# Kernel tuning notes

Hardware: AMD Instinct MI355X
Metric: run time of the kernel (lower is better)

Reference implementation:

```python
import jax, jax.numpy as jnp
import numpy as np

HID = 100

def _make_params(key):
    dims = [(2, HID), (HID, HID), (HID, HID), (HID, HID), (HID, 2)]
    params = {}
    for i, (fan_in, fan_out) in enumerate(dims):
        k1, k2, key = jax.random.split(key, 3)
        bound = 1.0 / np.sqrt(fan_in)
        params[f"W{i+1}"] = jax.random.uniform(k1, (fan_out, fan_in), jnp.float32, -bound, bound)
        params[f"b{i+1}"] = jax.random.uniform(k2, (fan_out,), jnp.float32, -bound, bound)
    return params

def setup_inputs() -> dict:
    key = jax.random.key(0)
    kx, kt, kp = jax.random.split(key, 3)
    N = 262144
    inp = {
        "x": jax.random.normal(kx, (N, 1), jnp.float32),
        "t": jax.random.uniform(kt, (N, 1), jnp.float32),
    }
    inp.update(_make_params(kp))
    return inp

def reference(x, t, W1, b1, W2, b2, W3, b3, W4, b4, W5, b5):
    hidden = [(W1, b1), (W2, b2), (W3, b3), (W4, b4)]

    def u(xs, ts):  # scalar xs, ts -> [2] = (u_r, u_i)
        h = jnp.stack([xs, ts])
        for W, b in hidden:
            h = jnp.tanh(W @ h + b)
        return W5 @ h + b5

    u_t = jax.jacfwd(u, argnums=1)          # [2]: (u_t_r, u_t_i)
    u_x = jax.jacfwd(u, argnums=0)          # [2]
    u_xx = jax.jacfwd(u_x, argnums=0)       # [2]: (u_xx_r, u_xx_i)

    def per_point(xs, ts):
        return u(xs, ts), u_t(xs, ts), u_xx(xs, ts)

    U, Ut, Uxx = jax.vmap(per_point)(x[:, 0], t[:, 0])  # each [N, 2]

    u_r, u_i = U[:, 0:1], U[:, 1:2]
    u_t_r, u_t_i = Ut[:, 0:1], Ut[:, 1:2]
    u_xx_r, u_xx_i = Uxx[:, 0:1], Uxx[:, 1:2]

    mag2 = u_r * u_r + u_i * u_i
    f_r = -u_t_i + 0.5 * u_xx_r + mag2 * u_r
    f_i = u_t_r + 0.5 * u_xx_i + mag2 * u_i
    return f_r, f_i
```

## Files before the change

### kernel.cpp

```cpp
#include <hip/hip_runtime.h>


using half8 = __attribute__((ext_vector_type(8))) _Float16;
using half4 = __attribute__((ext_vector_type(4))) _Float16;
using f32x4 = __attribute__((ext_vector_type(4))) float;

#define LW      44800
#define ZOFF    134400
#define STGOFF  134416
#define STGW    2304
#define PLANEB  1152
#define NWAVES  12
#define SMEM_BYTES 162064

union U8 { uint4 u; half8 h; };
union U4 { uint2 u; half4 h; };

static __device__ __forceinline__ float fast_tanh(float z) {
    float e = __expf(2.0f * z);
    return 1.0f - 2.0f * __builtin_amdgcn_rcpf(e + 1.0f);
}

static __device__ __forceinline__ void split2(float v, _Float16& h0, _Float16& h1) {
    h0 = (_Float16)v;
    h1 = (_Float16)((v - (float)h0) * 512.0f);
}

__global__ void prep_w(const float* __restrict__ W2, const float* __restrict__ W3,
                       const float* __restrict__ W4, unsigned short* __restrict__ ws) {
    int bid = blockIdx.x;
    int l = bid / 28, rem = bid % 28, kt = rem / 7, jt = rem % 7;
    const float* W = (l == 0) ? W2 : (l == 1) ? W3 : W4;
    int lane = threadIdx.x;
    int c = lane & 15, q = lane >> 4;
    int j = 16 * jt + c;
    if (kt < 3) {
        for (int s = 0; s < 2; ++s)
            for (int i = 0; i < 8; ++i) {
                int k = 32 * kt + 8 * q + i;
                float w = (j < 100) ? W[j * 100 + k] : 0.0f;
                _Float16 h0 = (_Float16)w;
                _Float16 val = (s == 0) ? h0 : (_Float16)((w - (float)h0) * 512.0f);
                ws[(l*LW + kt*14336 + jt*2048 + s*1024 + lane*16 + i*2) >> 1] =
                    __builtin_bit_cast(unsigned short, val);
            }
    } else if (lane < 16) {
        for (int s = 0; s < 2; ++s)
            for (int i = 0; i < 4; ++i) {
                int k = 96 + i;
                float w = (j < 100) ? W[j * 100 + k] : 0.0f;
                _Float16 h0 = (_Float16)w;
                _Float16 val = (s == 0) ? h0 : (_Float16)((w - (float)h0) * 512.0f);
                ws[(l*LW + 43008 + jt*256 + s*128 + lane*8 + i*2) >> 1] =
                    __builtin_bit_cast(unsigned short, val);
            }
    }
}

__global__ void __launch_bounds__(768) pinn_mfma(
    const float* __restrict__ x,  const float* __restrict__ t,
    const float* __restrict__ W1, const float* __restrict__ b1,
    const float* __restrict__ b2, const float* __restrict__ b3,
    const float* __restrict__ b4,
    const float* __restrict__ W5, const float* __restrict__ b5,
    const char* __restrict__ ws, float* __restrict__ out,
    int N, int nchunks)
{
    extern __shared__ char smem[];
    const int tid  = threadIdx.x;
    const int w    = tid >> 6;
    const int lane = tid & 63;
    const int c15  = lane & 15;
    const int q    = lane >> 4;

    for (int it = 0; it < 11; ++it) {
        int idx = tid + it * 768;
        if (idx < 8400) ((uint4*)smem)[idx] = ((const uint4*)ws)[idx];
    }
    if (tid < 4) *(unsigned*)(smem + ZOFF + tid * 4) = 0u;
    __syncthreads();

    char* stg = smem + STGOFF + w * STGW;

    half8 a0[3], a1[3];
    half4 a0t,   a1t;
    f32x4 c0[7], c1[7];

    for (int chunk = blockIdx.x; chunk < nchunks; chunk += gridDim.x) {
        const int colbase = chunk * 192 + w * 16;

        {
            int col = colbase + c15;
            int pt = col >> 2, ch = col & 3;
            int ptc = (pt < N) ? pt : (N - 1);
            float xv = x[ptc], tv = t[ptc];
            #pragma unroll
            for (int kt = 0; kt < 3; ++kt) {
                half8 v0, v1;
                #pragma unroll
                for (int i = 0; i < 8; ++i) {
                    int j = 32 * kt + 8 * q + i;
                    float w0 = W1[2*j], w1 = W1[2*j+1], bb = b1[j];
                    float p = fmaf(w0, xv, fmaf(w1, tv, bb));
                    float a = fast_tanh(p);
                    float s = 1.0f - a * a;
                    float v = (ch == 0) ? a : (ch == 1) ? s * w1
                             : (ch == 2) ? s * w0 : -2.0f * a * s * w0 * w0;
                    _Float16 h0, h1; split2(v, h0, h1);
                    v0[i] = h0; v1[i] = h1;
                }
                a0[kt] = v0; a1[kt] = v1;
            }
            half4 t0 = {0, 0, 0, 0}, t1 = {0, 0, 0, 0};
            if (q == 0) {
                #pragma unroll
                for (int i = 0; i < 4; ++i) {
                    int j = 96 + i;
                    float w0 = W1[2*j], w1 = W1[2*j+1], bb = b1[j];
                    float p = fmaf(w0, xv, fmaf(w1, tv, bb));
                    float a = fast_tanh(p);
                    float s = 1.0f - a * a;
                    float v = (ch == 0) ? a : (ch == 1) ? s * w1
                             : (ch == 2) ? s * w0 : -2.0f * a * s * w0 * w0;
                    _Float16 h0, h1; split2(v, h0, h1);
                    t0[i] = h0; t1[i] = h1;
                }
            }
            a0t = t0; a1t = t1;
        }

        for (int l = 0; l < 3; ++l) {
            const char* WL = smem + l * LW;
            const float* BL = (l == 0) ? b2 : (l == 1) ? b3 : b4;

            #pragma unroll
            for (int jt = 0; jt < 7; ++jt) {
                c0[jt] = (f32x4){0.f, 0.f, 0.f, 0.f};
                c1[jt] = (f32x4){0.f, 0.f, 0.f, 0.f};
            }

            #pragma unroll
            for (int kt = 0; kt < 3; ++kt)
                #pragma unroll
                for (int jt = 0; jt < 7; ++jt) {
                    U8 b0u, b1u;
                    b0u.u = *(const uint4*)(WL + kt*14336 + jt*2048 + lane*16);
                    b1u.u = *(const uint4*)(WL + kt*14336 + jt*2048 + 1024 + lane*16);
                    c0[jt] = __builtin_amdgcn_mfma_f32_16x16x32_f16(a0[kt], b0u.h, c0[jt], 0, 0, 0);
                    c1[jt] = __builtin_amdgcn_mfma_f32_16x16x32_f16(a0[kt], b1u.h, c1[jt], 0, 0, 0);
                    c1[jt] = __builtin_amdgcn_mfma_f32_16x16x32_f16(a1[kt], b0u.h, c1[jt], 0, 0, 0);
                }
            #pragma unroll
            for (int jt = 0; jt < 7; ++jt) {
                int toff  = (lane < 16) ? (l*LW + 43008 + jt*256 + lane*8) : ZOFF;
                int toff1 = (lane < 16) ? (toff + 128) : ZOFF;
                U4 b0u, b1u;
                b0u.u = *(const uint2*)(smem + toff);
                b1u.u = *(const uint2*)(smem + toff1);
                c0[jt] = __builtin_amdgcn_mfma_f32_16x16x16f16(a0t, b0u.h, c0[jt], 0, 0, 0);
                c1[jt] = __builtin_amdgcn_mfma_f32_16x16x16f16(a0t, b1u.h, c1[jt], 0, 0, 0);
                c1[jt] = __builtin_amdgcn_mfma_f32_16x16x16f16(a1t, b0u.h, c1[jt], 0, 0, 0);
            }

            if (l < 2) {
                #pragma unroll
                for (int kc = 0; kc < 4; ++kc) {
                    int njt = (kc < 3) ? 2 : 1;
                    #pragma unroll
                    for (int jj = 0; jj < 2; ++jj) {
                        if (jj >= njt) continue;
                        int jt = 2 * kc + jj;
                        int kk = 16 * jj + c15;
                        int j  = 16 * jt + c15;
                        float bj = BL[(j < 100) ? j : 99];
                        float z0 = c0[jt][0] + c1[jt][0] * (1.0f/512.0f) + bj;
                        float z1 = c0[jt][1] + c1[jt][1] * (1.0f/512.0f);
                        float z2 = c0[jt][2] + c1[jt][2] * (1.0f/512.0f);
                        float z3 = c0[jt][3] + c1[jt][3] * (1.0f/512.0f);
                        float a = fast_tanh(z0);
                        float s = 1.0f - a * a;
                        float v[4];
                        v[0] = a; v[1] = s * z1; v[2] = s * z2;
                        v[3] = fmaf(-2.0f * a * s * z2, z2, s * z3);
                        #pragma unroll
                        for (int r = 0; r < 4; ++r) {
                            _Float16 h0, h1; split2(v[r], h0, h1);
                            _Float16* bp = (_Float16*)(stg) + (4 * q + r) * 36 + kk;
                            bp[0]   = h0;
                            bp[576] = h1;
                        }
                    }
                    if (kc < 3) {
                        const char* rb = stg + c15 * 72 + 16 * q;
                        U8 u;
                        uint2 L, H;
                        L = *(const uint2*)(rb);              H = *(const uint2*)(rb + 8);
                        u.u = (uint4){L.x, L.y, H.x, H.y};    a0[kc] = u.h;
                        L = *(const uint2*)(rb + PLANEB);     H = *(const uint2*)(rb + PLANEB + 8);
                        u.u = (uint4){L.x, L.y, H.x, H.y};    a1[kc] = u.h;
                    } else {
                        U4 u;
                        if (q == 0) {
                            const char* rb = stg + c15 * 72;
                            u.u = *(const uint2*)(rb);            a0t = u.h;
                            u.u = *(const uint2*)(rb + PLANEB);   a1t = u.h;
                        } else {
                            a0t = (half4){0,0,0,0}; a1t = (half4){0,0,0,0};
                        }
                    }
                }
            } else {
                float p00 = 0.f, p01 = 0.f, p03 = 0.f;
                float p10 = 0.f, p11 = 0.f, p13 = 0.f;
                #pragma unroll
                for (int jt = 0; jt < 7; ++jt) {
                    int j = 16 * jt + c15;
                    int j2 = (j < 100) ? j : 99;
                    float m = (j < 100) ? 1.0f : 0.0f;
                    float bj = BL[j2];
                    float w50 = W5[j2] * m, w51 = W5[100 + j2] * m;
                    float z0 = c0[jt][0] + c1[jt][0] * (1.0f/512.0f) + bj;
                    float z1 = c0[jt][1] + c1[jt][1] * (1.0f/512.0f);
                    float z2 = c0[jt][2] + c1[jt][2] * (1.0f/512.0f);
                    float z3 = c0[jt][3] + c1[jt][3] * (1.0f/512.0f);
                    float a = fast_tanh(z0);
                    float s = 1.0f - a * a;
                    float v0 = a, v1 = s * z1;
                    float v3 = fmaf(-2.0f * a * s * z2, z2, s * z3);
                    p00 = fmaf(w50, v0, p00);
                    p01 = fmaf(w50, v1, p01);
                    p03 = fmaf(w50, v3, p03);
                    p10 = fmaf(w51, v0, p10);
                    p11 = fmaf(w51, v1, p11);
                    p13 = fmaf(w51, v3, p13);
                }
                #pragma unroll
                for (int m = 1; m <= 8; m <<= 1) {
                    p00 += __shfl_xor(p00, m, 64);
                    p01 += __shfl_xor(p01, m, 64);
                    p03 += __shfl_xor(p03, m, 64);
                    p10 += __shfl_xor(p10, m, 64);
                    p11 += __shfl_xor(p11, m, 64);
                    p13 += __shfl_xor(p13, m, 64);
                }
                int pt = chunk * 48 + w * 4 + q;
                if (c15 == 0 && pt < N) {
                    float ur = p00 + b5[0], ui = p10 + b5[1];
                    float mag2 = ur * ur + ui * ui;
                    float fr = fmaf(mag2, ur, fmaf(0.5f, p03, -p11));
                    float fi = fmaf(mag2, ui, fmaf(0.5f, p13,  p01));
                    out[pt]     = fr;
                    out[N + pt] = fi;
                }
            }
        }
    }
}

extern "C" void kernel_launch(void* const* d_in, const int* in_sizes, int n_in,
                              void* d_out, int out_size, void* d_ws, size_t ws_size,
                              hipStream_t stream) {
    const float* x  = (const float*)d_in[0];
    const float* t  = (const float*)d_in[1];
    const float* W1 = (const float*)d_in[2];
    const float* b1 = (const float*)d_in[3];
    const float* W2 = (const float*)d_in[4];
    const float* b2 = (const float*)d_in[5];
    const float* W3 = (const float*)d_in[6];
    const float* b3 = (const float*)d_in[7];
    const float* W4 = (const float*)d_in[8];
    const float* b4 = (const float*)d_in[9];
    const float* W5 = (const float*)d_in[10];
    const float* b5 = (const float*)d_in[11];
    float* out = (float*)d_out;
    const int N = in_sizes[0];
    const int nchunks = (N + 47) / 48;

    (void)hipFuncSetAttribute((const void*)pinn_mfma,
                              hipFuncAttributeMaxDynamicSharedMemorySize, SMEM_BYTES);

    prep_w<<<84, 64, 0, stream>>>(W2, W3, W4, (unsigned short*)d_ws);
    pinn_mfma<<<256, 768, SMEM_BYTES, stream>>>(x, t, W1, b1, b2, b3, b4, W5, b5,
                                                (const char*)d_ws, out, N, nchunks);
}
```

Before: 436.1 us.

## Read MFMA weights directly from global memory instead of staging in LDS

Removes the per-block copy of all three hidden-layer weight matrices (about 134 KB) into shared memory. MFMA B operands are now loaded straight from the global workspace, relying on L1/L2 caching. Blocks shrink from 12 waves to 4, and the launch grows to 2048 blocks with an occupancy hint, so more independent waves can hide load latency. The cost is more global/cache traffic per MFMA and possible L1 thrashing, since every wave repeatedly reloads the same weights.

```diff
diff --git a/kernel.cpp b/kernel.cpp
--- a/kernel.cpp
+++ b/kernel.cpp
@@ -6,12 +6,9 @@
 using f32x4 = __attribute__((ext_vector_type(4))) float;
 
 #define LW      44800
-#define ZOFF    134400
-#define STGOFF  134416
 #define STGW    2304
 #define PLANEB  1152
-#define NWAVES  12
-#define SMEM_BYTES 162064
+#define NWAVES  4
 
 union U8 { uint4 u; half8 h; };
 union U4 { uint2 u; half4 h; };
@@ -57,7 +54,7 @@
     }
 }
 
-__global__ void __launch_bounds__(768) pinn_mfma(
+__global__ void __launch_bounds__(256, 5) pinn_mfma(
     const float* __restrict__ x,  const float* __restrict__ t,
     const float* __restrict__ W1, const float* __restrict__ b1,
     const float* __restrict__ b2, const float* __restrict__ b3,
@@ -66,28 +63,21 @@
     const char* __restrict__ ws, float* __restrict__ out,
     int N, int nchunks)
 {
-    extern __shared__ char smem[];
+    __shared__ __align__(16) char smem[NWAVES * STGW];
     const int tid  = threadIdx.x;
     const int w    = tid >> 6;
     const int lane = tid & 63;
     const int c15  = lane & 15;
     const int q    = lane >> 4;
 
-    for (int it = 0; it < 11; ++it) {
-        int idx = tid + it * 768;
-        if (idx < 8400) ((uint4*)smem)[idx] = ((const uint4*)ws)[idx];
-    }
-    if (tid < 4) *(unsigned*)(smem + ZOFF + tid * 4) = 0u;
-    __syncthreads();
-
-    char* stg = smem + STGOFF + w * STGW;
+    char* stg = smem + w * STGW;
 
     half8 a0[3], a1[3];
     half4 a0t,   a1t;
     f32x4 c0[7], c1[7];
 
     for (int chunk = blockIdx.x; chunk < nchunks; chunk += gridDim.x) {
-        const int colbase = chunk * 192 + w * 16;
+        const int colbase = chunk * 64 + w * 16;
 
         {
             int col = colbase + c15;
@@ -130,7 +120,7 @@
         }
 
         for (int l = 0; l < 3; ++l) {
-            const char* WL = smem + l * LW;
+            const char* WL = ws + l * LW;
             const float* BL = (l == 0) ? b2 : (l == 1) ? b3 : b4;
 
             #pragma unroll
@@ -152,11 +142,14 @@
                 }
             #pragma unroll
             for (int jt = 0; jt < 7; ++jt) {
-                int toff  = (lane < 16) ? (l*LW + 43008 + jt*256 + lane*8) : ZOFF;
-                int toff1 = (lane < 16) ? (toff + 128) : ZOFF;
                 U4 b0u, b1u;
-                b0u.u = *(const uint2*)(smem + toff);
-                b1u.u = *(const uint2*)(smem + toff1);
+                b0u.u = (uint2){0u, 0u};
+                b1u.u = (uint2){0u, 0u};
+                if (lane < 16) {
+                    const char* tp = WL + 43008 + jt*256 + lane*8;
+                    b0u.u = *(const uint2*)(tp);
+                    b1u.u = *(const uint2*)(tp + 128);
+                }
                 c0[jt] = __builtin_amdgcn_mfma_f32_16x16x16f16(a0t, b0u.h, c0[jt], 0, 0, 0);
                 c1[jt] = __builtin_amdgcn_mfma_f32_16x16x16f16(a0t, b1u.h, c1[jt], 0, 0, 0);
                 c1[jt] = __builtin_amdgcn_mfma_f32_16x16x16f16(a1t, b0u.h, c1[jt], 0, 0, 0);
@@ -243,7 +236,7 @@
                     p11 += __shfl_xor(p11, m, 64);
                     p13 += __shfl_xor(p13, m, 64);
                 }
-                int pt = chunk * 48 + w * 4 + q;
+                int pt = chunk * 16 + w * 4 + q;
                 if (c15 == 0 && pt < N) {
                     float ur = p00 + b5[0], ui = p10 + b5[1];
                     float mag2 = ur * ur + ui * ui;
@@ -274,12 +267,9 @@
     const float* b5 = (const float*)d_in[11];
     float* out = (float*)d_out;
     const int N = in_sizes[0];
-    const int nchunks = (N + 47) / 48;
-
-    (void)hipFuncSetAttribute((const void*)pinn_mfma,
-                              hipFuncAttributeMaxDynamicSharedMemorySize, SMEM_BYTES);
+    const int nchunks = (N + 15) / 16;
 
     prep_w<<<84, 64, 0, stream>>>(W2, W3, W4, (unsigned short*)d_ws);
-    pinn_mfma<<<256, 768, SMEM_BYTES, stream>>>(x, t, W1, b1, b2, b3, b4, W5, b5,
-                                                (const char*)d_ws, out, N, nchunks);
-}
+    pinn_mfma<<<2048, 256, 0, stream>>>(x, t, W1, b1, b2, b3, b4, W5, b5,
+                                        (const char*)d_ws, out, N, nchunks);
+}
```

Result: slower. 1.135 ms (+160.4%).

## Split layer GEMM into two column groups and raise block to 16 waves

Applied to the files above, without the earlier changes.

Each layer's 7 output tiles are now computed in two groups (4 then 3). Each group's accumulators are consumed right away: activation, fp16 split and a write to a smaller per-wave staging window, from which the next layer's A fragments are gathered into separate registers. This lowers the peak count of live accumulator registers, which allows 1024-thread blocks (16 waves, 64 points per chunk) instead of 768. The risk is more register pressure from the extra n0/n1 fragment arrays, and more LDS traffic and redundant 16-byte reads in the new staging layout.

```diff
diff --git a/kernel.cpp b/kernel.cpp
--- a/kernel.cpp
+++ b/kernel.cpp
@@ -7,11 +7,11 @@
 
 #define LW      44800
 #define ZOFF    134400
-#define STGOFF  134416
-#define STGW    2304
-#define PLANEB  1152
-#define NWAVES  12
-#define SMEM_BYTES 162064
+#define WINOFF  134416
+#define WINW    1536
+#define ROWB    48
+#define PLANEB2 768
+#define SMEM_BYTES 158992
 
 union U8 { uint4 u; half8 h; };
 union U4 { uint2 u; half4 h; };
@@ -57,7 +57,7 @@
     }
 }
 
-__global__ void __launch_bounds__(768) pinn_mfma(
+__global__ void __launch_bounds__(1024) pinn_mfma(
     const float* __restrict__ x,  const float* __restrict__ t,
     const float* __restrict__ W1, const float* __restrict__ b1,
     const float* __restrict__ b2, const float* __restrict__ b3,
@@ -73,21 +73,22 @@
     const int c15  = lane & 15;
     const int q    = lane >> 4;
 
-    for (int it = 0; it < 11; ++it) {
-        int idx = tid + it * 768;
+    for (int it = 0; it < 9; ++it) {
+        int idx = tid + it * 1024;
         if (idx < 8400) ((uint4*)smem)[idx] = ((const uint4*)ws)[idx];
     }
     if (tid < 4) *(unsigned*)(smem + ZOFF + tid * 4) = 0u;
     __syncthreads();
 
-    char* stg = smem + STGOFF + w * STGW;
+    char* win = smem + WINOFF + w * WINW;
 
     half8 a0[3], a1[3];
     half4 a0t,   a1t;
-    f32x4 c0[7], c1[7];
+    half8 n0[3], n1[3];
+    half4 n0t,   n1t;
 
     for (int chunk = blockIdx.x; chunk < nchunks; chunk += gridDim.x) {
-        const int colbase = chunk * 192 + w * 16;
+        const int colbase = chunk * 256 + w * 16;
 
         {
             int col = colbase + c15;
@@ -133,107 +134,148 @@
             const char* WL = smem + l * LW;
             const float* BL = (l == 0) ? b2 : (l == 1) ? b3 : b4;
 
-            #pragma unroll
-            for (int jt = 0; jt < 7; ++jt) {
-                c0[jt] = (f32x4){0.f, 0.f, 0.f, 0.f};
-                c1[jt] = (f32x4){0.f, 0.f, 0.f, 0.f};
-            }
-
-            #pragma unroll
-            for (int kt = 0; kt < 3; ++kt)
-                #pragma unroll
-                for (int jt = 0; jt < 7; ++jt) {
-                    U8 b0u, b1u;
-                    b0u.u = *(const uint4*)(WL + kt*14336 + jt*2048 + lane*16);
-                    b1u.u = *(const uint4*)(WL + kt*14336 + jt*2048 + 1024 + lane*16);
-                    c0[jt] = __builtin_amdgcn_mfma_f32_16x16x32_f16(a0[kt], b0u.h, c0[jt], 0, 0, 0);
-                    c1[jt] = __builtin_amdgcn_mfma_f32_16x16x32_f16(a0[kt], b1u.h, c1[jt], 0, 0, 0);
-                    c1[jt] = __builtin_amdgcn_mfma_f32_16x16x32_f16(a1[kt], b0u.h, c1[jt], 0, 0, 0);
-                }
-            #pragma unroll
-            for (int jt = 0; jt < 7; ++jt) {
-                int toff  = (lane < 16) ? (l*LW + 43008 + jt*256 + lane*8) : ZOFF;
-                int toff1 = (lane < 16) ? (toff + 128) : ZOFF;
-                U4 b0u, b1u;
-                b0u.u = *(const uint2*)(smem + toff);
-                b1u.u = *(const uint2*)(smem + toff1);
-                c0[jt] = __builtin_amdgcn_mfma_f32_16x16x16f16(a0t, b0u.h, c0[jt], 0, 0, 0);
-                c1[jt] = __builtin_amdgcn_mfma_f32_16x16x16f16(a0t, b1u.h, c1[jt], 0, 0, 0);
-                c1[jt] = __builtin_amdgcn_mfma_f32_16x16x16f16(a1t, b0u.h, c1[jt], 0, 0, 0);
-            }
+            float p00 = 0.f, p01 = 0.f, p03 = 0.f;
+            float p10 = 0.f, p11 = 0.f, p13 = 0.f;
+
+            #define CONSUME(JT, C0, C1)                                          \
+            {                                                                    \
+                int j  = 16 * (JT) + c15;                                        \
+                float z0 = (C0)[0] + (C1)[0] * (1.0f/512.0f);                    \
+                float z1 = (C0)[1] + (C1)[1] * (1.0f/512.0f);                    \
+                float z2 = (C0)[2] + (C1)[2] * (1.0f/512.0f);                    \
+                float z3 = (C0)[3] + (C1)[3] * (1.0f/512.0f);                    \
+                if (l < 2) {                                                     \
+                    float bj = BL[(j < 100) ? j : 99];                           \
+                    float a = fast_tanh(z0 + bj);                                \
+                    float s = 1.0f - a * a;                                      \
+                    float v0 = a, v1 = s * z1, v2 = s * z2;                      \
+                    float v3 = fmaf(-2.0f * a * s * z2, z2, s * z3);             \
+                    _Float16 h0, h1;                                             \
+                    char* bp = win + c15 * 2;                                    \
+                    split2(v0, h0, h1);                                          \
+                    *(_Float16*)(bp + (4*q+0)*ROWB) = h0;                        \
+                    *(_Float16*)(bp + (4*q+0)*ROWB + PLANEB2) = h1;              \
+                    split2(v1, h0, h1);                                          \
+                    *(_Float16*)(bp + (4*q+1)*ROWB) = h0;                        \
+                    *(_Float16*)(bp + (4*q+1)*ROWB + PLANEB2) = h1;              \
+                    split2(v2, h0, h1);                                          \
+                    *(_Float16*)(bp + (4*q+2)*ROWB) = h0;                        \
+                    *(_Float16*)(bp + (4*q+2)*ROWB + PLANEB2) = h1;              \
+                    split2(v3, h0, h1);                                          \
+                    *(_Float16*)(bp + (4*q+3)*ROWB) = h0;                        \
+                    *(_Float16*)(bp + (4*q+3)*ROWB + PLANEB2) = h1;              \
+                    if ((JT) < 6) {                                              \
+                        const int nidx = ((JT) < 6) ? ((JT) >> 1) : 0;           \
+                        const char* rb = win + c15 * ROWB + (q & 1) * 16;        \
+                        U8 mu8;                                                  \
+                        bool act = ((q >> 1) == ((JT) & 1));                     \
+                        mu8.u = *(const uint4*)(rb);                             \
+                        if (act) n0[nidx] = mu8.h;                               \
+                        mu8.u = *(const uint4*)(rb + PLANEB2);                   \
+                        if (act) n1[nidx] = mu8.h;                               \
+                    } else {                                                     \
+                        const char* rb = win + c15 * ROWB;                       \
+                        U4 mu4;                                                  \
+                        mu4.u = *(const uint2*)(rb);                             \
+                        n0t = (q == 0) ? mu4.h : (half4){0,0,0,0};               \
+                        mu4.u = *(const uint2*)(rb + PLANEB2);                   \
+                        n1t = (q == 0) ? mu4.h : (half4){0,0,0,0};               \
+                    }                                                            \
+                } else {                                                         \
+                    int j2 = (j < 100) ? j : 99;                                 \
+                    float m = (j < 100) ? 1.0f : 0.0f;                           \
+                    float bj = BL[j2];                                           \
+                    float w50 = W5[j2] * m, w51 = W5[100 + j2] * m;              \
+                    float a = fast_tanh(z0 + bj);                                \
+                    float s = 1.0f - a * a;                                      \
+                    float v0 = a, v1 = s * z1;                                   \
+                    float v3 = fmaf(-2.0f * a * s * z2, z2, s * z3);             \
+                    p00 = fmaf(w50, v0, p00);                                    \
+                    p01 = fmaf(w50, v1, p01);                                    \
+                    p03 = fmaf(w50, v3, p03);                                    \
+                    p10 = fmaf(w51, v0, p10);                                    \
+                    p11 = fmaf(w51, v1, p11);                                    \
+                    p13 = fmaf(w51, v3, p13);                                    \
+                }                                                                \
+            }
+
+            {
+                f32x4 c0[4], c1[4];
+                #pragma unroll
+                for (int u = 0; u < 4; ++u) {
+                    c0[u] = (f32x4){0.f, 0.f, 0.f, 0.f};
+                    c1[u] = (f32x4){0.f, 0.f, 0.f, 0.f};
+                }
+                #pragma unroll
+                for (int kt = 0; kt < 3; ++kt)
+                    #pragma unroll
+                    for (int u = 0; u < 4; ++u) {
+                        U8 b0u, b1u;
+                        b0u.u = *(const uint4*)(WL + kt*14336 + u*2048 + lane*16);
+                        b1u.u = *(const uint4*)(WL + kt*14336 + u*2048 + 1024 + lane*16);
+                        c0[u] = __builtin_amdgcn_mfma_f32_16x16x32_f16(a0[kt], b0u.h, c0[u], 0, 0, 0);
+                        c1[u] = __builtin_amdgcn_mfma_f32_16x16x32_f16(a0[kt], b1u.h, c1[u], 0, 0, 0);
+                        c1[u] = __builtin_amdgcn_mfma_f32_16x16x32_f16(a1[kt], b0u.h, c1[u], 0, 0, 0);
+                    }
+                #pragma unroll
+                for (int u = 0; u < 4; ++u) {
+                    int toff  = (lane < 16) ? (l*LW + 43008 + u*256 + lane*8) : ZOFF;
+                    int toff1 = (lane < 16) ? (toff + 128) : ZOFF;
+                    U4 b0u, b1u;
+                    b0u.u = *(const uint2*)(smem + toff);
+                    b1u.u = *(const uint2*)(smem + toff1);
+                    c0[u] = __builtin_amdgcn_mfma_f32_16x16x16f16(a0t, b0u.h, c0[u], 0, 0, 0);
+                    c1[u] = __builtin_amdgcn_mfma_f32_16x16x16f16(a0t, b1u.h, c1[u], 0, 0, 0);
+                    c1[u] = __builtin_amdgcn_mfma_f32_16x16x16f16(a1t, b0u.h, c1[u], 0, 0, 0);
+                }
+                CONSUME(0, c0[0], c1[0]);
+                CONSUME(1, c0[1], c1[1]);
+                CONSUME(2, c0[2], c1[2]);
+                CONSUME(3, c0[3], c1[3]);
+            }
+
+            {
+                f32x4 c0[3], c1[3];
+                #pragma unroll
+                for (int u = 0; u < 3; ++u) {
+                    c0[u] = (f32x4){0.f, 0.f, 0.f, 0.f};
+                    c1[u] = (f32x4){0.f, 0.f, 0.f, 0.f};
+                }
+                #pragma unroll
+                for (int kt = 0; kt < 3; ++kt)
+                    #pragma unroll
+                    for (int u = 0; u < 3; ++u) {
+                        int jt = 4 + u;
+                        U8 b0u, b1u;
+                        b0u.u = *(const uint4*)(WL + kt*14336 + jt*2048 + lane*16);
+                        b1u.u = *(const uint4*)(WL + kt*14336 + jt*2048 + 1024 + lane*16);
+                        c0[u] = __builtin_amdgcn_mfma_f32_16x16x32_f16(a0[kt], b0u.h, c0[u], 0, 0, 0);
+                        c1[u] = __builtin_amdgcn_mfma_f32_16x16x32_f16(a0[kt], b1u.h, c1[u], 0, 0, 0);
+                        c1[u] = __builtin_amdgcn_mfma_f32_16x16x32_f16(a1[kt], b0u.h, c1[u], 0, 0, 0);
+                    }
+                #pragma unroll
+                for (int u = 0; u < 3; ++u) {
+                    int jt = 4 + u;
+                    int toff  = (lane < 16) ? (l*LW + 43008 + jt*256 + lane*8) : ZOFF;
+                    int toff1 = (lane < 16) ? (toff + 128) : ZOFF;
+                    U4 b0u, b1u;
+                    b0u.u = *(const uint2*)(smem + toff);
+                    b1u.u = *(const uint2*)(smem + toff1);
+                    c0[u] = __builtin_amdgcn_mfma_f32_16x16x16f16(a0t, b0u.h, c0[u], 0, 0, 0);
+                    c1[u] = __builtin_amdgcn_mfma_f32_16x16x16f16(a0t, b1u.h, c1[u], 0, 0, 0);
+                    c1[u] = __builtin_amdgcn_mfma_f32_16x16x16f16(a1t, b0u.h, c1[u], 0, 0, 0);
+                }
+                CONSUME(4, c0[0], c1[0]);
+                CONSUME(5, c0[1], c1[1]);
+                CONSUME(6, c0[2], c1[2]);
+            }
+            #undef CONSUME
 
             if (l < 2) {
-                #pragma unroll
-                for (int kc = 0; kc < 4; ++kc) {
-                    int njt = (kc < 3) ? 2 : 1;
-                    #pragma unroll
-                    for (int jj = 0; jj < 2; ++jj) {
-                        if (jj >= njt) continue;
-                        int jt = 2 * kc + jj;
-                        int kk = 16 * jj + c15;
-                        int j  = 16 * jt + c15;
-                        float bj = BL[(j < 100) ? j : 99];
-                        float z0 = c0[jt][0] + c1[jt][0] * (1.0f/512.0f) + bj;
-                        float z1 = c0[jt][1] + c1[jt][1] * (1.0f/512.0f);
-                        float z2 = c0[jt][2] + c1[jt][2] * (1.0f/512.0f);
-                        float z3 = c0[jt][3] + c1[jt][3] * (1.0f/512.0f);
-                        float a = fast_tanh(z0);
-                        float s = 1.0f - a * a;
-                        float v[4];
-                        v[0] = a; v[1] = s * z1; v[2] = s * z2;
-                        v[3] = fmaf(-2.0f * a * s * z2, z2, s * z3);
-                        #pragma unroll
-                        for (int r = 0; r < 4; ++r) {
-                            _Float16 h0, h1; split2(v[r], h0, h1);
-                            _Float16* bp = (_Float16*)(stg) + (4 * q + r) * 36 + kk;
-                            bp[0]   = h0;
-                            bp[576] = h1;
-                        }
-                    }
-                    if (kc < 3) {
-                        const char* rb = stg + c15 * 72 + 16 * q;
-                        U8 u;
-                        uint2 L, H;
-                        L = *(const uint2*)(rb);              H = *(const uint2*)(rb + 8);
-                        u.u = (uint4){L.x, L.y, H.x, H.y};    a0[kc] = u.h;
-                        L = *(const uint2*)(rb + PLANEB);     H = *(const uint2*)(rb + PLANEB + 8);
-                        u.u = (uint4){L.x, L.y, H.x, H.y};    a1[kc] = u.h;
-                    } else {
-                        U4 u;
-                        if (q == 0) {
-                            const char* rb = stg + c15 * 72;
-                            u.u = *(const uint2*)(rb);            a0t = u.h;
-                            u.u = *(const uint2*)(rb + PLANEB);   a1t = u.h;
-                        } else {
-                            a0t = (half4){0,0,0,0}; a1t = (half4){0,0,0,0};
-                        }
-                    }
-                }
+                a0[0] = n0[0]; a0[1] = n0[1]; a0[2] = n0[2];
+                a1[0] = n1[0]; a1[1] = n1[1]; a1[2] = n1[2];
+                a0t = n0t; a1t = n1t;
             } else {
-                float p00 = 0.f, p01 = 0.f, p03 = 0.f;
-                float p10 = 0.f, p11 = 0.f, p13 = 0.f;
-                #pragma unroll
-                for (int jt = 0; jt < 7; ++jt) {
-                    int j = 16 * jt + c15;
-                    int j2 = (j < 100) ? j : 99;
-                    float m = (j < 100) ? 1.0f : 0.0f;
-                    float bj = BL[j2];
-                    float w50 = W5[j2] * m, w51 = W5[100 + j2] * m;
-                    float z0 = c0[jt][0] + c1[jt][0] * (1.0f/512.0f) + bj;
-                    float z1 = c0[jt][1] + c1[jt][1] * (1.0f/512.0f);
-                    float z2 = c0[jt][2] + c1[jt][2] * (1.0f/512.0f);
-                    float z3 = c0[jt][3] + c1[jt][3] * (1.0f/512.0f);
-                    float a = fast_tanh(z0);
-                    float s = 1.0f - a * a;
-                    float v0 = a, v1 = s * z1;
-                    float v3 = fmaf(-2.0f * a * s * z2, z2, s * z3);
-                    p00 = fmaf(w50, v0, p00);
-                    p01 = fmaf(w50, v1, p01);
-                    p03 = fmaf(w50, v3, p03);
-                    p10 = fmaf(w51, v0, p10);
-                    p11 = fmaf(w51, v1, p11);
-                    p13 = fmaf(w51, v3, p13);
-                }
                 #pragma unroll
                 for (int m = 1; m <= 8; m <<= 1) {
                     p00 += __shfl_xor(p00, m, 64);
@@ -243,7 +285,7 @@
                     p11 += __shfl_xor(p11, m, 64);
                     p13 += __shfl_xor(p13, m, 64);
                 }
-                int pt = chunk * 48 + w * 4 + q;
+                int pt = chunk * 64 + w * 4 + q;
                 if (c15 == 0 && pt < N) {
                     float ur = p00 + b5[0], ui = p10 + b5[1];
                     float mag2 = ur * ur + ui * ui;
@@ -274,12 +316,12 @@
     const float* b5 = (const float*)d_in[11];
     float* out = (float*)d_out;
     const int N = in_sizes[0];
-    const int nchunks = (N + 47) / 48;
+    const int nchunks = (N + 63) / 64;
 
     (void)hipFuncSetAttribute((const void*)pinn_mfma,
                               hipFuncAttributeMaxDynamicSharedMemorySize, SMEM_BYTES);
 
     prep_w<<<84, 64, 0, stream>>>(W2, W3, W4, (unsigned short*)d_ws);
-    pinn_mfma<<<256, 768, SMEM_BYTES, stream>>>(x, t, W1, b1, b2, b3, b4, W5, b5,
-                                                (const char*)d_ws, out, N, nchunks);
-}
+    pinn_mfma<<<256, 1024, SMEM_BYTES, stream>>>(x, t, W1, b1, b2, b3, b4, W5, b5,
+                                                 (const char*)d_ws, out, N, nchunks);
+}
```

After: 663.5 us. +52.1%, slower.
